# Kernel optimization log

Measured on AMD Instinct MI355X. Metric: run time of the kernel, lower is better.

The kernel has to match this reference:

```python
import jax, jax.numpy as jnp
import numpy as np

N, E, F_IN, C = 50000, 800000, 128, 300
NEG_SLOPE = 0.2  # PyG GATv2Conv default negative_slope


def setup_inputs() -> dict:
    key = jax.random.key(0)
    ks = jax.random.split(key, 10)
    x = jax.random.normal(ks[0], (N, F_IN), dtype=jnp.float32)
    edge_index = jax.random.randint(ks[1], (2, E), 0, N, dtype=jnp.int64)
    s_in = np.float32(1.0 / np.sqrt(F_IN))
    s_c = np.float32(1.0 / np.sqrt(C))
    Wl = jax.random.normal(ks[2], (F_IN, C), dtype=jnp.float32) * s_in
    bl = jnp.zeros((C,), jnp.float32)
    Wr = jax.random.normal(ks[3], (F_IN, C), dtype=jnp.float32) * s_in
    br = jnp.zeros((C,), jnp.float32)
    att = jax.random.normal(ks[4], (C,), dtype=jnp.float32) * s_c
    bias = jnp.zeros((C,), jnp.float32)
    lw = jax.random.normal(ks[5], (C, 1), dtype=jnp.float32) * s_c
    lb = jnp.zeros((1,), jnp.float32)
    return {"x": x, "edge_index": edge_index, "Wl": Wl, "bl": bl,
            "Wr": Wr, "br": br, "att": att, "bias": bias, "lw": lw, "lb": lb}


def reference(x, edge_index, Wl, bl, Wr, br, att, bias, lw, lb):
    n = x.shape[0]
    # GATv2: separate source/target linear transforms
    xl = x @ Wl + bl  # [N, C] (source / message features)
    xr = x @ Wr + br  # [N, C] (target features)
    # add self loops (PyG default add_self_loops=True)
    loops = jnp.arange(n, dtype=edge_index.dtype)
    src = jnp.concatenate([edge_index[0], loops])  # [E+N]
    dst = jnp.concatenate([edge_index[1], loops])  # [E+N]
    # GATv2 attention logit: a^T LeakyReLU(xl_j + xr_i)
    e = jax.nn.leaky_relu(xl[src] + xr[dst], NEG_SLOPE) @ att  # [E+N]
    # segment softmax over incoming edges of each target node
    m = jax.ops.segment_max(e, dst, num_segments=n)
    ex = jnp.exp(e - m[dst])
    denom = jax.ops.segment_sum(ex, dst, num_segments=n)
    alpha = ex / denom[dst]  # [E+N]
    # weighted scatter-aggregation of source messages + conv bias
    out = jax.ops.segment_sum(xl[src] * alpha[:, None], dst, num_segments=n) + bias
    h = jax.nn.relu(out)          # torch.relu
    # F.dropout in eval mode is identity (reference is inference math)
    return jax.nn.sigmoid(h @ lw + lb)  # [N, 1]
```

## Files before the change

### kernel.cpp

```cpp
#include <hip/hip_runtime.h>
#include <hip/hip_fp16.h>

#define F_IN 128
#define C_DIM 300
#define NEG_SLOPE 0.2f
#define NCT  40
#define CH   8
#define NPB  256

typedef _Float16 half8 __attribute__((ext_vector_type(8)));
typedef _Float16 half4 __attribute__((ext_vector_type(4)));
typedef _Float16 h2    __attribute__((ext_vector_type(2)));
typedef float    f32x4 __attribute__((ext_vector_type(4)));
typedef float    f32x2 __attribute__((ext_vector_type(2)));

__device__ inline h2 as_h2(unsigned u) { union { unsigned u; h2 h; } c; c.u = u; return c.h; }
__device__ inline unsigned as_u(h2 h)  { union { unsigned u; h2 h; } c; c.h = h; return c.u; }
__device__ inline f32x2 upv(unsigned u) {
    h2 h = as_h2(u);
    f32x2 r; r.x = (float)h.x; r.y = (float)h.y; return r;
}

#if __has_builtin(__builtin_amdgcn_fdot2)
__device__ inline float fdot2w(h2 a, h2 b, float c) {
    return __builtin_amdgcn_fdot2(a, b, c, false);
}
#else
__device__ inline float fdot2w(h2 a, h2 b, float c) {
    return fmaf((float)a.y, (float)b.y, fmaf((float)a.x, (float)b.x, c));
}
#endif

__global__ __launch_bounds__(256) void convert_w(
    const float* __restrict__ Wl, const float* __restrict__ Wr,
    _Float16* __restrict__ Bp)
{
    int idx = blockIdx.x * 256 + threadIdx.x;
    if (idx >= 640 * F_IN) return;
    int nn = idx % 640;
    int k  = idx / 640;
    float v = 0.f;
    if (nn < 300)                   v = Wl[k * C_DIM + nn];
    else if (nn >= 304 && nn < 604) v = Wr[k * C_DIM + (nn - 304)];
    int ct = nn >> 4, n16 = nn & 15;
    int kr = k & 31,  ks  = k >> 5;
    int lane = ((kr >> 3) << 4) | n16;
    int j = k & 7;
    Bp[((((ct * 4 + ks) * 64) + lane) << 3) | j] = (_Float16)v;
}

__global__ __launch_bounds__(256) void gemm_xlxr(
    const float* __restrict__ x, const _Float16* __restrict__ Bp,
    const float* __restrict__ bl, const float* __restrict__ br,
    _Float16* __restrict__ xlh, _Float16* __restrict__ xrh, int n)
{
    __shared__ __align__(16) _Float16 xs[64][136];
    const int rb0 = blockIdx.x * 64;
    const int t   = threadIdx.x;

    #pragma unroll
    for (int i = 0; i < 8; ++i) {
        int flat = (i * 256 + t) * 4;
        int r = flat >> 7;
        int k = flat & 127;
        int gr = rb0 + r;
        if (gr >= n) gr = n - 1;
        float4 v = *reinterpret_cast<const float4*>(x + (size_t)gr * F_IN + k);
        half4 h = { (_Float16)v.x, (_Float16)v.y, (_Float16)v.z, (_Float16)v.w };
        *reinterpret_cast<half4*>(&xs[r][k]) = h;
    }
    __syncthreads();

    const int w    = t >> 6;
    const int lane = t & 63;
    const int m    = lane & 15;
    const int quad = lane >> 4;

    half8 a[4];
    #pragma unroll
    for (int ks = 0; ks < 4; ++ks)
        a[ks] = *reinterpret_cast<const half8*>(&xs[w * 16 + m][ks * 32 + quad * 8]);

    const int rbase = rb0 + w * 16 + quad * 4;

    #pragma unroll 4
    for (int ct = 0; ct < NCT; ++ct) {
        f32x4 acc = {0.f, 0.f, 0.f, 0.f};
        #pragma unroll
        for (int ks = 0; ks < 4; ++ks) {
            half8 b = *reinterpret_cast<const half8*>(
                Bp + (((size_t)(ct * 4 + ks) * 64 + lane) << 3));
            acc = __builtin_amdgcn_mfma_f32_16x16x32_f16(a[ks], b, acc, 0, 0, 0);
        }
        int col = ct * 16 + m;
        int isL = (col < 300);
        int isR = (col >= 304 && col < 604);
        if (isL | isR) {
            float bv = isL ? bl[col] : br[col - 304];
            _Float16* tab = isL ? (xlh + col) : (xrh + (col - 304));
            #pragma unroll
            for (int reg = 0; reg < 4; ++reg) {
                int row = rbase + reg;
                if (row < n)
                    tab[(size_t)row * C_DIM] = (_Float16)(acc[reg] + bv);
            }
        }
    }
}

__global__ __launch_bounds__(256) void bucket_count(
    const int* __restrict__ dst, unsigned* __restrict__ bcnt, int nE, int chunk)
{
    __shared__ unsigned cnt[256];
    const int b = blockIdx.x, t = threadIdx.x;
    cnt[t] = 0;
    __syncthreads();
    const int lo = b * chunk;
    const int hi = min(nE, lo + chunk);
    for (int i = lo + t; i < hi; i += 256)
        atomicAdd(&cnt[dst[i] >> 8], 1u);
    __syncthreads();
    bcnt[t * NPB + b] = cnt[t];
}

__global__ __launch_bounds__(256) void scan_part(
    const unsigned* __restrict__ counts, unsigned* __restrict__ bsum, int n)
{
    __shared__ unsigned s[256];
    const int t = threadIdx.x;
    const int base = blockIdx.x * 1024 + t * 4;
    unsigned v = 0;
    #pragma unroll
    for (int i = 0; i < 4; ++i) {
        int idx = base + i;
        if (idx < n) v += counts[idx];
    }
    s[t] = v;
    __syncthreads();
    for (int off = 128; off > 0; off >>= 1) {
        if (t < off) s[t] += s[t + off];
        __syncthreads();
    }
    if (t == 0) bsum[blockIdx.x] = s[0];
}

__global__ __launch_bounds__(64) void scan_mid(
    unsigned* __restrict__ bsum, unsigned* __restrict__ offs, int nblk, int n)
{
    const int lane = threadIdx.x;
    unsigned v = (lane < nblk) ? bsum[lane] : 0u;
    unsigned inc = v;
    #pragma unroll
    for (int off = 1; off < 64; off <<= 1) {
        unsigned u = __shfl_up(inc, off);
        if (lane >= off) inc += u;
    }
    if (lane < nblk) bsum[lane] = inc - v;
    if (lane == 63) offs[n] = inc;
}

__global__ __launch_bounds__(256) void scan_final(
    const unsigned* __restrict__ counts, const unsigned* __restrict__ bsum,
    unsigned* __restrict__ offs, unsigned* __restrict__ cursor, int n)
{
    __shared__ unsigned s[256];
    const int t = threadIdx.x;
    const int base = blockIdx.x * 1024 + t * 4;
    unsigned c[4];
    unsigned v = 0;
    #pragma unroll
    for (int i = 0; i < 4; ++i) {
        int idx = base + i;
        c[i] = (idx < n) ? counts[idx] : 0u;
        v += c[i];
    }
    s[t] = v;
    __syncthreads();
    for (int off = 1; off < 256; off <<= 1) {
        unsigned u = (t >= off) ? s[t - off] : 0u;
        __syncthreads();
        if (t >= off) s[t] += u;
        __syncthreads();
    }
    unsigned run = bsum[blockIdx.x] + s[t] - v;
    #pragma unroll
    for (int i = 0; i < 4; ++i) {
        int idx = base + i;
        if (idx < n) {
            offs[idx] = run;
            cursor[idx] = run;
            run += c[i];
        }
    }
}

__global__ __launch_bounds__(256) void partition_edges(
    const int* __restrict__ src, const int* __restrict__ dst,
    const unsigned* __restrict__ boff,
    int* __restrict__ ebuf_src, int* __restrict__ ebuf_dst, int nE, int chunk)
{
    __shared__ unsigned cur[256];
    const int b = blockIdx.x, t = threadIdx.x;
    cur[t] = boff[t * NPB + b];
    __syncthreads();
    const int lo = b * chunk;
    const int hi = min(nE, lo + chunk);
    for (int i = lo + t; i < hi; i += 256) {
        int d  = dst[i];
        int sv = src[i];
        unsigned p = atomicAdd(&cur[d >> 8], 1u);
        ebuf_src[p] = sv;
        ebuf_dst[p] = d;
    }
}

__global__ __launch_bounds__(256) void bucket_csr(
    const int* __restrict__ ebuf_src, const int* __restrict__ ebuf_dst,
    const unsigned* __restrict__ boff, unsigned* __restrict__ offs,
    int* __restrict__ csr_src, int n, int nE, int nb)
{
    __shared__ unsigned cnt[256];
    __shared__ unsigned s[256];
    __shared__ unsigned cur[256];
    const int bk = blockIdx.x;
    const int t  = threadIdx.x;
    const unsigned bstart = boff[(unsigned)bk * NPB];
    const unsigned bend   = boff[(unsigned)(bk + 1) * NPB];
    cnt[t] = 0;
    __syncthreads();
    for (unsigned i = bstart + t; i < bend; i += 256)
        atomicAdd(&cnt[ebuf_dst[i] & 255], 1u);
    __syncthreads();
    unsigned v = cnt[t];
    s[t] = v;
    __syncthreads();
    for (int off = 1; off < 256; off <<= 1) {
        unsigned u = (t >= off) ? s[t - off] : 0u;
        __syncthreads();
        if (t >= off) s[t] += u;
        __syncthreads();
    }
    const unsigned excl = s[t] - v;
    const int node = (bk << 8) + t;
    if (node <= n) offs[node] = bstart + excl;
    if (t == 0 && bk == nb - 1 && (n & 255) == 0) offs[n] = (unsigned)nE;
    cur[t] = bstart + excl;
    __syncthreads();
    for (unsigned i = bstart + t; i < bend; i += 256) {
        int d = ebuf_dst[i];
        unsigned p = atomicAdd(&cur[d & 255], 1u);
        csr_src[p] = ebuf_src[i];
    }
}

__global__ __launch_bounds__(256) void gat_gather(
    const int* __restrict__ csr_src, const unsigned* __restrict__ offs,
    const _Float16* __restrict__ xlh, const _Float16* __restrict__ xrh,
    const float* __restrict__ att, const float* __restrict__ bias,
    const float* __restrict__ lw, const float* __restrict__ lb,
    float* __restrict__ y, int n)
{
    __shared__ __align__(16) float lds[4 * 560];
    float* part = lds + (threadIdx.x >> 6) * 560;

    const int wid  = (blockIdx.x * blockDim.x + threadIdx.x) >> 6;
    const int lane = threadIdx.x & 63;
    if (wid >= n) return;

    const int l2   = 2 * lane;
    const bool has2 = (lane < 22);
    const int t8   = lane & 7;
    const int o    = lane >> 3;
    const int byteoff = lane * 4;

    const _Float16* xrrow = xrh + (size_t)wid * C_DIM;
    h2 xr0 = *(const h2*)(xrrow + l2);
    h2 xr1 = *(const h2*)(xrrow + 128 + l2);
    h2 xr2 = {(_Float16)0, (_Float16)0};
    if (has2) xr2 = *(const h2*)(xrrow + 256 + l2);

    h2 a06[3], a04[3];
    #pragma unroll
    for (int k = 0; k < 3; ++k) {
        int c = 128 * k + l2;
        float ax = (c < C_DIM) ? att[c] : 0.f;
        float ay = (c + 1 < C_DIM) ? att[c + 1] : 0.f;
        a06[k].x = (_Float16)(0.6f * ax); a06[k].y = (_Float16)(0.6f * ay);
        a04[k].x = (_Float16)(0.4f * ax); a04[k].y = (_Float16)(0.4f * ay);
    }

    f32x2 acc2[3] = {{0.f, 0.f}, {0.f, 0.f}, {0.f, 0.f}};
    float den_l = 0.f;

    const unsigned start = offs[wid];
    const int totalE = (int)(offs[wid + 1] - start) + 1;
    const char* basep = (const char*)xlh;

    for (int base = 0; base < totalE; base += CH) {
        int idv = wid;
        {
            int k = base + lane;
            if (lane < CH && k > 0 && k < totalE) idv = csr_src[start + k - 1];
        }
        int rowb = idv * (C_DIM * 2);
        int ro[CH];
        #pragma unroll
        for (int tt = 0; tt < CH; ++tt) ro[tt] = __shfl(rowb, tt);

        unsigned pk0[CH], pk1[CH], pk2[CH];
        #pragma unroll
        for (int tt = 0; tt < CH; ++tt) {
            const char* p = basep + ro[tt] + byteoff;
            pk0[tt] = *(const unsigned*)(p);
            pk1[tt] = *(const unsigned*)(p + 256);
            pk2[tt] = 0u;
        }
        if (has2) {
            #pragma unroll
            for (int tt = 0; tt < CH; ++tt)
                pk2[tt] = *(const unsigned*)(basep + ro[tt] + byteoff + 512);
        }

        #pragma unroll
        for (int tt = 0; tt < CH; ++tt) {
            h2 z0 = as_h2(pk0[tt]) + xr0;
            h2 z1 = as_h2(pk1[tt]) + xr1;
            h2 z2 = as_h2(pk2[tt]) + xr2;
            float p = fdot2w(z0, a06[0], 0.f);
            p = fdot2w(as_h2(as_u(z0) & 0x7FFF7FFFu), a04[0], p);
            p = fdot2w(z1, a06[1], p);
            p = fdot2w(as_h2(as_u(z1) & 0x7FFF7FFFu), a04[1], p);
            p = fdot2w(z2, a06[2], p);
            p = fdot2w(as_h2(as_u(z2) & 0x7FFF7FFFu), a04[2], p);
            part[tt * 68 + lane] = p;
        }

        float wgt;
        {
            const int oo = (o + t8) & 7;
            const float* rp = part + t8 * 68 + oo * 8;
            float4 s0 = *(const float4*)(rp + 0);
            float4 s1 = *(const float4*)(rp + 4);
            float e = ((s0.x + s0.y) + (s0.z + s0.w)) + ((s1.x + s1.y) + (s1.z + s1.w));
            e += __shfl_xor(e, 8);
            e += __shfl_xor(e, 16);
            e += __shfl_xor(e, 32);
            bool valid = (base + t8) < totalE;
            wgt = valid ? __expf(fminf(e, 60.f)) : 0.f;
        }

        den_l += wgt;

        _Float16 wh = (_Float16)wgt;
        h2 wpair = {wh, wh};
        unsigned wbits = as_u(wpair);
        h2 hacc0 = {(_Float16)0, (_Float16)0};
        h2 hacc1 = {(_Float16)0, (_Float16)0};
        h2 hacc2 = {(_Float16)0, (_Float16)0};
        #pragma unroll
        for (int tt = 0; tt < CH; ++tt) {
            h2 wt2 = as_h2(__shfl(wbits, tt));
            hacc0 += wt2 * as_h2(pk0[tt]);
            hacc1 += wt2 * as_h2(pk1[tt]);
            hacc2 += wt2 * as_h2(pk2[tt]);
        }
        acc2[0] += upv(as_u(hacc0));
        acc2[1] += upv(as_u(hacc1));
        acc2[2] += upv(as_u(hacc2));
    }

    float den = den_l;
    den += __shfl_xor(den, 1);
    den += __shfl_xor(den, 2);
    den += __shfl_xor(den, 4);

    const float invd = 1.f / den;
    float dot = 0.f;
    #pragma unroll
    for (int k = 0; k < 3; ++k) {
        #pragma unroll
        for (int j = 0; j < 2; ++j) {
            int c = 128 * k + l2 + j;
            float b = (c < C_DIM) ? bias[c] : 0.f;
            float l = (c < C_DIM) ? lw[c] : 0.f;
            float a = (j == 0) ? acc2[k].x : acc2[k].y;
            float h = fmaf(a, invd, b);
            h = h > 0.f ? h : 0.f;
            dot = fmaf(h, l, dot);
        }
    }
    #pragma unroll
    for (int off = 32; off; off >>= 1) dot += __shfl_xor(dot, off);
    if (lane == 0) y[wid] = 1.f / (1.f + __expf(-(dot + lb[0])));
}

extern "C" void kernel_launch(void* const* d_in, const int* in_sizes, int n_in,
                              void* d_out, int out_size, void* d_ws, size_t ws_size,
                              hipStream_t stream)
{
    const float* x    = (const float*)d_in[0];
    const int*   ei   = (const int*)d_in[1];
    const float* Wl   = (const float*)d_in[2];
    const float* bl   = (const float*)d_in[3];
    const float* Wr   = (const float*)d_in[4];
    const float* br   = (const float*)d_in[5];
    const float* att  = (const float*)d_in[6];
    const float* bias = (const float*)d_in[7];
    const float* lw   = (const float*)d_in[8];
    const float* lb   = (const float*)d_in[9];
    float* y = (float*)d_out;

    const int n  = in_sizes[0] / F_IN;
    const int nE = in_sizes[1] / 2;
    const int* src_arr = ei;
    const int* dst_arr = ei + nE;

    const int NB    = (n + 255) >> 8;
    const int chunk = (nE + NPB - 1) / NPB;
    const int M     = 256 * NPB;
    const int nblkM = (M + 1023) / 1024;

    _Float16* xlh      = (_Float16*)d_ws;
    _Float16* xrh      = xlh + (size_t)n * C_DIM;
    _Float16* Bp       = xrh + (size_t)n * C_DIM;
    unsigned* bcnt     = (unsigned*)(Bp + NCT * 4 * 64 * 8);
    unsigned* boff     = bcnt + M;
    unsigned* offs     = boff + (M + 1);
    unsigned* bsum     = offs + (n + 1);
    int*      csr_src  = (int*)(bsum + 64);
    int*      ebuf_src = csr_src + nE;
    int*      ebuf_dst = ebuf_src + nE;

    convert_w<<<(640 * F_IN + 255) / 256, 256, 0, stream>>>(Wl, Wr, Bp);

    bucket_count<<<NPB, 256, 0, stream>>>(dst_arr, bcnt, nE, chunk);
    scan_part<<<nblkM, 256, 0, stream>>>(bcnt, bsum, M);
    scan_mid<<<1, 64, 0, stream>>>(bsum, boff, nblkM, M);
    scan_final<<<nblkM, 256, 0, stream>>>(bcnt, bsum, boff, (unsigned*)ebuf_dst, M);
    partition_edges<<<NPB, 256, 0, stream>>>(src_arr, dst_arr, boff, ebuf_src, ebuf_dst, nE, chunk);
    bucket_csr<<<NB, 256, 0, stream>>>(ebuf_src, ebuf_dst, boff, offs, csr_src, n, nE, NB);

    gemm_xlxr<<<(n + 63) / 64, 256, 0, stream>>>(x, Bp, bl, br, xlh, xrh, n);

    gat_gather<<<(n + 3) / 4, 256, 0, stream>>>(csr_src, offs, xlh, xrh, att, bias, lw, lb, y, n);
}
```

Baseline: 259.4 us.

## Double-buffer gather loads, pack edge buffer, fold scan_mid into scan_final

The attention gather loop now software-pipelines: it issues the next chunk's row loads into a second register set while computing the current chunk, to hide gather latency. The CSR build packs each edge's 16-bit source id and low 8 dst bits into one word, halving partition/bucket traffic. The separate single-block scan_mid launch is removed; each scan_final block recomputes the 64-entry block-sum prefix itself. Costs are extra registers (possible occupancy loss) and a packing scheme that assumes fewer than 65536 nodes.

```diff
diff --git a/kernel.cpp b/kernel.cpp
--- a/kernel.cpp
+++ b/kernel.cpp
@@ -144,27 +144,24 @@
     if (t == 0) bsum[blockIdx.x] = s[0];
 }
 
-__global__ __launch_bounds__(64) void scan_mid(
-    unsigned* __restrict__ bsum, unsigned* __restrict__ offs, int nblk, int n)
-{
-    const int lane = threadIdx.x;
-    unsigned v = (lane < nblk) ? bsum[lane] : 0u;
-    unsigned inc = v;
-    #pragma unroll
-    for (int off = 1; off < 64; off <<= 1) {
-        unsigned u = __shfl_up(inc, off);
-        if (lane >= off) inc += u;
-    }
-    if (lane < nblk) bsum[lane] = inc - v;
-    if (lane == 63) offs[n] = inc;
-}
-
 __global__ __launch_bounds__(256) void scan_final(
     const unsigned* __restrict__ counts, const unsigned* __restrict__ bsum,
-    unsigned* __restrict__ offs, unsigned* __restrict__ cursor, int n)
+    unsigned* __restrict__ offs, unsigned* __restrict__ cursor, int n, int nblk)
 {
     __shared__ unsigned s[256];
+    __shared__ unsigned sbase;
     const int t = threadIdx.x;
+    if (t < 64) {
+        unsigned v64 = (t < nblk) ? bsum[t] : 0u;
+        unsigned inc = v64;
+        #pragma unroll
+        for (int off = 1; off < 64; off <<= 1) {
+            unsigned u = __shfl_up(inc, off);
+            if (t >= off) inc += u;
+        }
+        if (t == (int)blockIdx.x) sbase = inc - v64;
+        if (blockIdx.x == gridDim.x - 1 && t == 63) offs[n] = inc;
+    }
     const int base = blockIdx.x * 1024 + t * 4;
     unsigned c[4];
     unsigned v = 0;
@@ -182,7 +179,7 @@
         if (t >= off) s[t] += u;
         __syncthreads();
     }
-    unsigned run = bsum[blockIdx.x] + s[t] - v;
+    unsigned run = sbase + s[t] - v;
     #pragma unroll
     for (int i = 0; i < 4; ++i) {
         int idx = base + i;
@@ -197,7 +194,7 @@
 __global__ __launch_bounds__(256) void partition_edges(
     const int* __restrict__ src, const int* __restrict__ dst,
     const unsigned* __restrict__ boff,
-    int* __restrict__ ebuf_src, int* __restrict__ ebuf_dst, int nE, int chunk)
+    unsigned* __restrict__ ebuf, int nE, int chunk)
 {
     __shared__ unsigned cur[256];
     const int b = blockIdx.x, t = threadIdx.x;
@@ -209,15 +206,13 @@
         int d  = dst[i];
         int sv = src[i];
         unsigned p = atomicAdd(&cur[d >> 8], 1u);
-        ebuf_src[p] = sv;
-        ebuf_dst[p] = d;
+        ebuf[p] = (unsigned)sv | ((unsigned)(d & 255) << 16);
     }
 }
 
 __global__ __launch_bounds__(256) void bucket_csr(
-    const int* __restrict__ ebuf_src, const int* __restrict__ ebuf_dst,
-    const unsigned* __restrict__ boff, unsigned* __restrict__ offs,
-    int* __restrict__ csr_src, int n, int nE, int nb)
+    const unsigned* __restrict__ ebuf, const unsigned* __restrict__ boff,
+    unsigned* __restrict__ offs, int* __restrict__ csr_src, int n, int nE, int nb)
 {
     __shared__ unsigned cnt[256];
     __shared__ unsigned s[256];
@@ -229,7 +224,7 @@
     cnt[t] = 0;
     __syncthreads();
     for (unsigned i = bstart + t; i < bend; i += 256)
-        atomicAdd(&cnt[ebuf_dst[i] & 255], 1u);
+        atomicAdd(&cnt[(ebuf[i] >> 16) & 255], 1u);
     __syncthreads();
     unsigned v = cnt[t];
     s[t] = v;
@@ -247,11 +242,78 @@
     cur[t] = bstart + excl;
     __syncthreads();
     for (unsigned i = bstart + t; i < bend; i += 256) {
-        int d = ebuf_dst[i];
-        unsigned p = atomicAdd(&cur[d & 255], 1u);
-        csr_src[p] = ebuf_src[i];
-    }
-}
+        unsigned e = ebuf[i];
+        unsigned p = atomicAdd(&cur[(e >> 16) & 255], 1u);
+        csr_src[p] = (int)(e & 0xFFFFu);
+    }
+}
+
+#define ISSUE_CHUNK(ROWB, P0, P1, P2)                                      \
+  {                                                                        \
+    int ro_[CH];                                                           \
+    _Pragma("unroll")                                                      \
+    for (int tt = 0; tt < CH; ++tt) ro_[tt] = __shfl((ROWB), tt);          \
+    _Pragma("unroll")                                                      \
+    for (int tt = 0; tt < CH; ++tt) {                                      \
+        const char* p_ = basep + ro_[tt] + byteoff;                        \
+        P0[tt] = *(const unsigned*)(p_);                                   \
+        P1[tt] = *(const unsigned*)(p_ + 256);                             \
+        P2[tt] = 0u;                                                       \
+    }                                                                      \
+    if (has2) {                                                            \
+        _Pragma("unroll")                                                  \
+        for (int tt = 0; tt < CH; ++tt)                                    \
+            P2[tt] = *(const unsigned*)(basep + ro_[tt] + byteoff + 512);  \
+    }                                                                      \
+  }
+
+#define COMPUTE_CHUNK(P0, P1, P2, BASEIDX)                                 \
+  {                                                                        \
+    _Pragma("unroll")                                                      \
+    for (int tt = 0; tt < CH; ++tt) {                                      \
+        h2 z0 = as_h2(P0[tt]) + xr0;                                       \
+        h2 z1 = as_h2(P1[tt]) + xr1;                                       \
+        h2 z2 = as_h2(P2[tt]) + xr2;                                       \
+        float p = fdot2w(z0, a06[0], 0.f);                                 \
+        p = fdot2w(as_h2(as_u(z0) & 0x7FFF7FFFu), a04[0], p);              \
+        p = fdot2w(z1, a06[1], p);                                         \
+        p = fdot2w(as_h2(as_u(z1) & 0x7FFF7FFFu), a04[1], p);              \
+        p = fdot2w(z2, a06[2], p);                                         \
+        p = fdot2w(as_h2(as_u(z2) & 0x7FFF7FFFu), a04[2], p);              \
+        part[tt * 68 + lane] = p;                                          \
+    }                                                                      \
+    float wgt;                                                             \
+    {                                                                      \
+        const int oo = (o + t8) & 7;                                       \
+        const float* rp = part + t8 * 68 + oo * 8;                         \
+        float4 s0 = *(const float4*)(rp + 0);                              \
+        float4 s1 = *(const float4*)(rp + 4);                              \
+        float e = ((s0.x + s0.y) + (s0.z + s0.w)) +                        \
+                  ((s1.x + s1.y) + (s1.z + s1.w));                         \
+        e += __shfl_xor(e, 8);                                             \
+        e += __shfl_xor(e, 16);                                            \
+        e += __shfl_xor(e, 32);                                            \
+        bool valid = ((BASEIDX) + t8) < totalE;                            \
+        wgt = valid ? __expf(fminf(e, 60.f)) : 0.f;                        \
+    }                                                                      \
+    den_l += wgt;                                                          \
+    _Float16 wh = (_Float16)wgt;                                           \
+    h2 wpair = {wh, wh};                                                   \
+    unsigned wbits = as_u(wpair);                                          \
+    h2 hacc0 = {(_Float16)0, (_Float16)0};                                 \
+    h2 hacc1 = {(_Float16)0, (_Float16)0};                                 \
+    h2 hacc2 = {(_Float16)0, (_Float16)0};                                 \
+    _Pragma("unroll")                                                      \
+    for (int tt = 0; tt < CH; ++tt) {                                      \
+        h2 wt2 = as_h2(__shfl(wbits, tt));                                 \
+        hacc0 += wt2 * as_h2(P0[tt]);                                      \
+        hacc1 += wt2 * as_h2(P1[tt]);                                      \
+        hacc2 += wt2 * as_h2(P2[tt]);                                      \
+    }                                                                      \
+    acc2[0] += upv(as_u(hacc0));                                           \
+    acc2[1] += upv(as_u(hacc1));                                           \
+    acc2[2] += upv(as_u(hacc2));                                           \
+  }
 
 __global__ __launch_bounds__(256) void gat_gather(
     const int* __restrict__ csr_src, const unsigned* __restrict__ offs,
@@ -296,77 +358,40 @@
     const int totalE = (int)(offs[wid + 1] - start) + 1;
     const char* basep = (const char*)xlh;
 
-    for (int base = 0; base < totalE; base += CH) {
+    auto rowbase = [&](int b) -> int {
         int idv = wid;
-        {
-            int k = base + lane;
-            if (lane < CH && k > 0 && k < totalE) idv = csr_src[start + k - 1];
-        }
-        int rowb = idv * (C_DIM * 2);
-        int ro[CH];
-        #pragma unroll
-        for (int tt = 0; tt < CH; ++tt) ro[tt] = __shfl(rowb, tt);
-
-        unsigned pk0[CH], pk1[CH], pk2[CH];
-        #pragma unroll
-        for (int tt = 0; tt < CH; ++tt) {
-            const char* p = basep + ro[tt] + byteoff;
-            pk0[tt] = *(const unsigned*)(p);
-            pk1[tt] = *(const unsigned*)(p + 256);
-            pk2[tt] = 0u;
-        }
-        if (has2) {
-            #pragma unroll
-            for (int tt = 0; tt < CH; ++tt)
-                pk2[tt] = *(const unsigned*)(basep + ro[tt] + byteoff + 512);
-        }
-
-        #pragma unroll
-        for (int tt = 0; tt < CH; ++tt) {
-            h2 z0 = as_h2(pk0[tt]) + xr0;
-            h2 z1 = as_h2(pk1[tt]) + xr1;
-            h2 z2 = as_h2(pk2[tt]) + xr2;
-            float p = fdot2w(z0, a06[0], 0.f);
-            p = fdot2w(as_h2(as_u(z0) & 0x7FFF7FFFu), a04[0], p);
-            p = fdot2w(z1, a06[1], p);
-            p = fdot2w(as_h2(as_u(z1) & 0x7FFF7FFFu), a04[1], p);
-            p = fdot2w(z2, a06[2], p);
-            p = fdot2w(as_h2(as_u(z2) & 0x7FFF7FFFu), a04[2], p);
-            part[tt * 68 + lane] = p;
-        }
-
-        float wgt;
-        {
-            const int oo = (o + t8) & 7;
-            const float* rp = part + t8 * 68 + oo * 8;
-            float4 s0 = *(const float4*)(rp + 0);
-            float4 s1 = *(const float4*)(rp + 4);
-            float e = ((s0.x + s0.y) + (s0.z + s0.w)) + ((s1.x + s1.y) + (s1.z + s1.w));
-            e += __shfl_xor(e, 8);
-            e += __shfl_xor(e, 16);
-            e += __shfl_xor(e, 32);
-            bool valid = (base + t8) < totalE;
-            wgt = valid ? __expf(fminf(e, 60.f)) : 0.f;
-        }
-
-        den_l += wgt;
-
-        _Float16 wh = (_Float16)wgt;
-        h2 wpair = {wh, wh};
-        unsigned wbits = as_u(wpair);
-        h2 hacc0 = {(_Float16)0, (_Float16)0};
-        h2 hacc1 = {(_Float16)0, (_Float16)0};
-        h2 hacc2 = {(_Float16)0, (_Float16)0};
-        #pragma unroll
-        for (int tt = 0; tt < CH; ++tt) {
-            h2 wt2 = as_h2(__shfl(wbits, tt));
-            hacc0 += wt2 * as_h2(pk0[tt]);
-            hacc1 += wt2 * as_h2(pk1[tt]);
-            hacc2 += wt2 * as_h2(pk2[tt]);
-        }
-        acc2[0] += upv(as_u(hacc0));
-        acc2[1] += upv(as_u(hacc1));
-        acc2[2] += upv(as_u(hacc2));
+        int k = b + lane;
+        if (lane < CH && k > 0 && k < totalE) idv = csr_src[start + k - 1];
+        return idv * (C_DIM * 2);
+    };
+
+    unsigned A0[CH], A1[CH], A2[CH], B0[CH], B1[CH], B2[CH];
+    {
+        int rb = rowbase(0);
+        ISSUE_CHUNK(rb, A0, A1, A2);
+    }
+    int base = 0;
+    for (;;) {
+        int nb = base + CH;
+        if (nb < totalE) {
+            int rb = rowbase(nb);
+            ISSUE_CHUNK(rb, B0, B1, B2);
+            COMPUTE_CHUNK(A0, A1, A2, base);
+        } else {
+            COMPUTE_CHUNK(A0, A1, A2, base);
+            break;
+        }
+        base = nb;
+        nb = base + CH;
+        if (nb < totalE) {
+            int rb = rowbase(nb);
+            ISSUE_CHUNK(rb, A0, A1, A2);
+            COMPUTE_CHUNK(B0, B1, B2, base);
+        } else {
+            COMPUTE_CHUNK(B0, B1, B2, base);
+            break;
+        }
+        base = nb;
     }
 
     float den = den_l;
@@ -427,18 +452,17 @@
     unsigned* boff     = bcnt + M;
     unsigned* offs     = boff + (M + 1);
     unsigned* bsum     = offs + (n + 1);
-    int*      csr_src  = (int*)(bsum + 64);
-    int*      ebuf_src = csr_src + nE;
-    int*      ebuf_dst = ebuf_src + nE;
+    unsigned* cursM    = bsum + 64;
+    int*      csr_src  = (int*)(cursM + M);
+    unsigned* ebuf     = (unsigned*)(csr_src + nE);
 
     convert_w<<<(640 * F_IN + 255) / 256, 256, 0, stream>>>(Wl, Wr, Bp);
 
     bucket_count<<<NPB, 256, 0, stream>>>(dst_arr, bcnt, nE, chunk);
     scan_part<<<nblkM, 256, 0, stream>>>(bcnt, bsum, M);
-    scan_mid<<<1, 64, 0, stream>>>(bsum, boff, nblkM, M);
-    scan_final<<<nblkM, 256, 0, stream>>>(bcnt, bsum, boff, (unsigned*)ebuf_dst, M);
-    partition_edges<<<NPB, 256, 0, stream>>>(src_arr, dst_arr, boff, ebuf_src, ebuf_dst, nE, chunk);
-    bucket_csr<<<NB, 256, 0, stream>>>(ebuf_src, ebuf_dst, boff, offs, csr_src, n, nE, NB);
+    scan_final<<<nblkM, 256, 0, stream>>>(bcnt, bsum, boff, cursM, M, nblkM);
+    partition_edges<<<NPB, 256, 0, stream>>>(src_arr, dst_arr, boff, ebuf, nE, chunk);
+    bucket_csr<<<NB, 256, 0, stream>>>(ebuf, boff, offs, csr_src, n, nE, NB);
 
     gemm_xlxr<<<(n + 63) / 64, 256, 0, stream>>>(x, Bp, bl, br, xlh, xrh, n);
 
```

Measured after the change: 263.4 us. No clear change (+1.5%).
